# Optimization experiments

Hardware: AMD Instinct MI355X
Metric: run time of the kernel (lower is better)

Reference implementation:

```python
import jax, jax.numpy as jnp
import numpy as np

N = 100_000   # nodes
E = 1_600_000  # edges (avg degree 16)
D_IN, D_HID, D_OUT = 128, 128, 64


def setup_inputs() -> dict:
    key = jax.random.key(0)
    k = jax.random.split(key, 6)
    x = jax.random.normal(k[0], (N, D_IN), dtype=jnp.float32)
    edge_index = jax.random.randint(k[1], (2, E), 0, N, dtype=jnp.int32)
    W1 = jax.random.normal(k[2], (D_IN, D_HID), dtype=jnp.float32) / np.sqrt(D_IN)
    b1 = jnp.zeros((D_HID,), dtype=jnp.float32)
    W2 = jax.random.normal(k[3], (D_HID, D_OUT), dtype=jnp.float32) / np.sqrt(D_HID)
    b2 = jnp.zeros((D_OUT,), dtype=jnp.float32)
    return {"x": x, "edge_index": edge_index, "W1": W1, "b1": b1, "W2": W2, "b2": b2}


def reference(x, edge_index, W1, b1, W2, b2):
    # GCNConv (PyG defaults): add self-loops, symmetric deg^-1/2 normalization,
    # linear transform then sum-aggregate over neighbors, then bias.
    loop = jnp.arange(N, dtype=edge_index.dtype)
    src = jnp.concatenate([edge_index[0], loop])  # [E+N]
    dst = jnp.concatenate([edge_index[1], loop])  # [E+N]

    deg = jax.ops.segment_sum(jnp.ones(src.shape, jnp.float32), dst, num_segments=N)
    inv_sqrt_deg = jnp.where(deg > 0, jax.lax.rsqrt(jnp.maximum(deg, 1.0)), 0.0)
    coef = (inv_sqrt_deg[src] * inv_sqrt_deg[dst])[:, None]  # [E+N, 1]

    def gcn_conv(h, W, b):
        h = h @ W                                   # [N, d_out]
        msg = h[src] * coef                          # gather + scale, [E+N, d_out]
        return jax.ops.segment_sum(msg, dst, num_segments=N) + b

    h = jax.nn.relu(gcn_conv(x, W1, b1))
    # dropout is identity in eval mode
    return gcn_conv(h, W2, b2)
```

## Files before the change

### kernel.cpp

```cpp
#include <hip/hip_runtime.h>

#define NN 100000
#define NE 1600000
#define DI 128
#define DH 128
#define DO 64
#define NBK 391
#define SLOT 5120
#define PAD 16
#define EPB 8192
#define NSB ((NE + EPB - 1) / EPB)

typedef unsigned int uint;
typedef unsigned short ushort;
typedef __bf16 bf16x8 __attribute__((ext_vector_type(8)));
typedef float f32x4 __attribute__((ext_vector_type(4)));

__device__ __forceinline__ float bf_lo(uint u) { return __uint_as_float(u << 16); }
__device__ __forceinline__ float bf_hi(uint u) { return __uint_as_float(u & 0xffff0000u); }
__device__ __forceinline__ ushort f2bf(float f) {
    uint u = __float_as_uint(f);
    uint r = u + 0x7fffu + ((u >> 16) & 1u);
    return (ushort)(r >> 16);
}

__global__ void k_prep(const float* __restrict__ W1, const float* __restrict__ W2,
                       ushort* __restrict__ w1t, ushort* __restrict__ w2t,
                       int* __restrict__ bcur) {
    int t = blockIdx.x * 256 + threadIdx.x;
    if (t < NBK) bcur[t * PAD] = t * SLOT;
    if (t < 128 * 128) {
        int c = t >> 7, k = t & 127;
        w1t[t] = f2bf(W1[k * 128 + c]);
    } else if (t < 128 * 128 + 64 * 128) {
        int u = t - 128 * 128;
        int c = u >> 7, k = u & 127;
        w2t[u] = f2bf(W2[k * 64 + c]);
    }
}

__global__ __launch_bounds__(512) void k_bscatter(const int* __restrict__ src,
                                                  const int* __restrict__ dst,
                                                  int* __restrict__ bcur,
                                                  uint* __restrict__ ebuf) {
    __shared__ uint stage[EPB];
    __shared__ ushort bktid[EPB];
    __shared__ int lcnt[NBK];
    __shared__ int loff[NBK];
    __shared__ int gbase[NBK];
    __shared__ int s[512];
    int t = threadIdx.x;
    int e0 = blockIdx.x * EPB;
    int n = min(EPB, NE - e0);
    for (int i = t; i < NBK; i += 512) lcnt[i] = 0;
    __syncthreads();
    for (int i = t; i < n; i += 512)
        atomicAdd(&lcnt[dst[e0 + i] >> 8], 1);
    __syncthreads();
    int myc = (t < NBK) ? lcnt[t] : 0;
    s[t] = myc;
    __syncthreads();
    for (int d = 1; d < 512; d <<= 1) {
        int a = (t >= d) ? s[t - d] : 0;
        __syncthreads();
        s[t] += a;
        __syncthreads();
    }
    if (t < NBK) {
        loff[t] = s[t] - myc;
        gbase[t] = atomicAdd(&bcur[t * PAD], myc);
        lcnt[t] = s[t] - myc;
    }
    __syncthreads();
    for (int i = t; i < n; i += 512) {
        int d = dst[e0 + i];
        int sv = src[e0 + i];
        int b = d >> 8;
        int p = atomicAdd(&lcnt[b], 1);
        stage[p] = ((uint)sv << 8) | (uint)(d & 255);
        bktid[p] = (ushort)b;
    }
    __syncthreads();
    for (int j = t; j < n; j += 512) {
        int b = bktid[j];
        ebuf[gbase[b] + (j - loff[b])] = stage[j];
    }
}

__global__ __launch_bounds__(256) void k_bfill(const uint* __restrict__ ebuf,
                                               const int* __restrict__ bcur,
                                               uint2* __restrict__ offdeg,
                                               float* __restrict__ inv,
                                               int* __restrict__ csr_src) {
    __shared__ int cnt[256];
    __shared__ int s[256];
    __shared__ int cur[256];
    int b = blockIdx.x, t = threadIdx.x;
    int ebeg = b * SLOT;
    int eend = bcur[b * PAD];
    cnt[t] = 0;
    __syncthreads();
    for (int e = ebeg + t; e < eend; e += 256)
        atomicAdd(&cnt[ebuf[e] & 255], 1);
    __syncthreads();
    int v = cnt[t];
    s[t] = v;
    __syncthreads();
    for (int d = 1; d < 256; d <<= 1) {
        int a = (t >= d) ? s[t - d] : 0;
        __syncthreads();
        s[t] += a;
        __syncthreads();
    }
    int beg = ebeg + s[t] - v;
    int node = b * 256 + t;
    if (node < NN) {
        offdeg[node] = make_uint2((uint)beg, (uint)v);
        inv[node] = rsqrtf((float)v + 1.0f);
    }
    cur[t] = beg;
    __syncthreads();
    for (int e = ebeg + t; e < eend; e += 256) {
        uint ed = ebuf[e];
        int p = atomicAdd(&cur[ed & 255], 1);
        csr_src[p] = (int)(ed >> 8);
    }
}

template <int N, bool ABF16>
__global__ __launch_bounds__(256) void k_gemm_mfma(const void* __restrict__ Ap,
                                                   const ushort* __restrict__ Wt,
                                                   const float* __restrict__ inv,
                                                   ushort* __restrict__ out) {
    int wid = threadIdx.x >> 6;
    int lane = threadIdx.x & 63;
    int r0 = (blockIdx.x * 4 + wid) * 32;
    if (r0 >= NN) return;
    int rlo = lane & 15, khi = lane >> 4;

    constexpr int CT = N / 16;
    f32x4 acc[2][CT] = {};

#pragma unroll
    for (int ks = 0; ks < 4; ++ks) {
        bf16x8 bf[CT];
#pragma unroll
        for (int ct = 0; ct < CT; ++ct)
            bf[ct] = *(const bf16x8*)(Wt + (ct * 16 + rlo) * 128 + ks * 32 + khi * 8);
#pragma unroll
        for (int rt = 0; rt < 2; ++rt) {
            int row = r0 + rt * 16 + rlo;
            bf16x8 af;
            if (ABF16) {
                af = *(const bf16x8*)((const ushort*)Ap + (size_t)row * 128 + ks * 32 + khi * 8);
            } else {
                const float* pa = (const float*)Ap + (size_t)row * 128 + ks * 32 + khi * 8;
                float4 f0 = *(const float4*)pa;
                float4 f1 = *(const float4*)(pa + 4);
                af[0] = (__bf16)f0.x; af[1] = (__bf16)f0.y;
                af[2] = (__bf16)f0.z; af[3] = (__bf16)f0.w;
                af[4] = (__bf16)f1.x; af[5] = (__bf16)f1.y;
                af[6] = (__bf16)f1.z; af[7] = (__bf16)f1.w;
            }
#pragma unroll
            for (int ct = 0; ct < CT; ++ct)
                acc[rt][ct] = __builtin_amdgcn_mfma_f32_16x16x32_bf16(af, bf[ct], acc[rt][ct], 0, 0, 0);
        }
    }
#pragma unroll
    for (int rt = 0; rt < 2; ++rt) {
        int rowb = r0 + rt * 16 + 4 * khi;
#pragma unroll
        for (int b = 0; b < 4; ++b) {
            float sc = inv[rowb + b];
#pragma unroll
            for (int ct = 0; ct < CT; ++ct)
                out[(size_t)(rowb + b) * N + ct * 16 + rlo] = f2bf(acc[rt][ct][b] * sc);
        }
    }
}

template <bool RELU>
__global__ void k_agg128(const uint2* __restrict__ offdeg, const int* __restrict__ csr,
                         const ushort* __restrict__ tab, const float* __restrict__ inv,
                         const float* __restrict__ bias, ushort* __restrict__ outb) {
    int wid = threadIdx.x >> 6, lane = threadIdx.x & 63;
    int node = blockIdx.x * (blockDim.x >> 6) + wid;
    if (node >= NN) return;
    uint2 od = offdeg[node];
    int beg = (int)od.x, end = beg + (int)od.y;
    const uint* t32 = (const uint*)tab;
    float a0 = 0.f, a1 = 0.f;
    int e = beg;
    for (; e + 3 < end; e += 4) {
        int s0 = csr[e], s1 = csr[e + 1], s2 = csr[e + 2], s3 = csr[e + 3];
        uint u0 = t32[(size_t)s0 * 64 + lane];
        uint u1 = t32[(size_t)s1 * 64 + lane];
        uint u2 = t32[(size_t)s2 * 64 + lane];
        uint u3 = t32[(size_t)s3 * 64 + lane];
        a0 += bf_lo(u0); a1 += bf_hi(u0);
        a0 += bf_lo(u1); a1 += bf_hi(u1);
        a0 += bf_lo(u2); a1 += bf_hi(u2);
        a0 += bf_lo(u3); a1 += bf_hi(u3);
    }
    for (; e < end; ++e) {
        int s = csr[e];
        uint u = t32[(size_t)s * 64 + lane];
        a0 += bf_lo(u); a1 += bf_hi(u);
    }
    float invd = inv[node];
    uint us = t32[(size_t)node * 64 + lane];
    float2 b = *(const float2*)(bias + lane * 2);
    float r0 = fmaf(invd, a0 + bf_lo(us), b.x);
    float r1 = fmaf(invd, a1 + bf_hi(us), b.y);
    if (RELU) { r0 = fmaxf(r0, 0.f); r1 = fmaxf(r1, 0.f); }
    uint packed = (uint)f2bf(r0) | ((uint)f2bf(r1) << 16);
    *(uint*)(outb + (size_t)node * 128 + lane * 2) = packed;
}

__global__ void k_agg64(const uint2* __restrict__ offdeg, const int* __restrict__ csr,
                        const ushort* __restrict__ tab, const float* __restrict__ inv,
                        const float* __restrict__ bias, float* __restrict__ out) {
    int wid = threadIdx.x >> 6, lane = threadIdx.x & 63;
    int node = blockIdx.x * (blockDim.x >> 6) + wid;
    if (node >= NN) return;
    uint2 od = offdeg[node];
    int beg = (int)od.x, end = beg + (int)od.y;
    float a0 = 0.f;
    int e = beg;
    for (; e + 3 < end; e += 4) {
        int s0 = csr[e], s1 = csr[e + 1], s2 = csr[e + 2], s3 = csr[e + 3];
        float h0 = __uint_as_float((uint)tab[(size_t)s0 * 64 + lane] << 16);
        float h1 = __uint_as_float((uint)tab[(size_t)s1 * 64 + lane] << 16);
        float h2 = __uint_as_float((uint)tab[(size_t)s2 * 64 + lane] << 16);
        float h3 = __uint_as_float((uint)tab[(size_t)s3 * 64 + lane] << 16);
        a0 += h0; a0 += h1; a0 += h2; a0 += h3;
    }
    for (; e < end; ++e) {
        int s = csr[e];
        a0 += __uint_as_float((uint)tab[(size_t)s * 64 + lane] << 16);
    }
    float invd = inv[node];
    float hs = __uint_as_float((uint)tab[(size_t)node * 64 + lane] << 16);
    out[(size_t)node * 64 + lane] = fmaf(invd, a0 + hs, bias[lane]);
}

extern "C" void kernel_launch(void* const* d_in, const int* in_sizes, int n_in,
                              void* d_out, int out_size, void* d_ws, size_t ws_size,
                              hipStream_t stream) {
    const float* x  = (const float*)d_in[0];
    const int* ei   = (const int*)d_in[1];
    const int* src  = ei;
    const int* dst  = ei + NE;
    const float* W1 = (const float*)d_in[2];
    const float* b1 = (const float*)d_in[3];
    const float* W2 = (const float*)d_in[4];
    const float* b2 = (const float*)d_in[5];
    float* out = (float*)d_out;

    uint2*  offdeg  = (uint2*)d_ws;
    float*  inv     = (float*)(offdeg + NN);
    int*    bcur    = (int*)(inv + 100004);
    int*    csr_src = bcur + NBK * PAD;
    ushort* w1t     = (ushort*)(csr_src + NBK * SLOT);
    ushort* w2t     = w1t + 128 * 128;
    ushort* h       = w2t + 64 * 128;
    ushort* hagg    = h + (size_t)NN * DH;
    ushort* h2      = hagg + (size_t)NN * DH;
    uint*   ebuf    = (uint*)h2;

    k_prep<<<96, 256, 0, stream>>>(W1, W2, w1t, w2t, bcur);
    k_bscatter<<<NSB, 512, 0, stream>>>(src, dst, bcur, ebuf);
    k_bfill<<<NBK, 256, 0, stream>>>(ebuf, bcur, offdeg, inv, csr_src);

    k_gemm_mfma<DH, false><<<(NN + 127) / 128, 256, 0, stream>>>(x, w1t, inv, h);
    k_agg128<true><<<NN / 4, 256, 0, stream>>>(offdeg, csr_src, h, inv, b1, hagg);

    k_gemm_mfma<DO, true><<<(NN + 127) / 128, 256, 0, stream>>>(hagg, w2t, inv, h2);
    k_agg64<<<NN / 4, 256, 0, stream>>>(offdeg, csr_src, h2, inv, b2, out);
}
```

Measured before the change: 244.3 us.

## Store features in 16-column slices and aggregate per slice for cache locality

Intermediate bf16 feature tables now use a column-sliced layout: 16-column slices, each covering all nodes contiguously. Both GEMMs read and write this layout, and the aggregation kernels run one slice per block. Each slice covers only a few MB, so the random neighbour gathers for that slice should stay in L2/MALL cache instead of thrashing across the full table. Within a wavefront, lanes are split into 8-lane feature groups and 4 edge subgroups per node, reduced with shuffles. In exchange, each gather is a 32-byte segment rather than a full 256-byte row, and the CSR indices are re-read once per slice.

```diff
diff --git a/kernel.cpp b/kernel.cpp
--- a/kernel.cpp
+++ b/kernel.cpp
@@ -5,6 +5,7 @@
 #define DI 128
 #define DH 128
 #define DO 64
+#define NN16 ((size_t)NN * 16)
 #define NBK 391
 #define SLOT 5120
 #define PAD 16
@@ -152,7 +153,9 @@
             int row = r0 + rt * 16 + rlo;
             bf16x8 af;
             if (ABF16) {
-                af = *(const bf16x8*)((const ushort*)Ap + (size_t)row * 128 + ks * 32 + khi * 8);
+                const ushort* As = (const ushort*)Ap;
+                af = *(const bf16x8*)(As + (size_t)(2 * ks + (khi >> 1)) * NN16 +
+                                      (size_t)row * 16 + (khi & 1) * 8);
             } else {
                 const float* pa = (const float*)Ap + (size_t)row * 128 + ks * 32 + khi * 8;
                 float4 f0 = *(const float4*)pa;
@@ -175,74 +178,103 @@
             float sc = inv[rowb + b];
 #pragma unroll
             for (int ct = 0; ct < CT; ++ct)
-                out[(size_t)(rowb + b) * N + ct * 16 + rlo] = f2bf(acc[rt][ct][b] * sc);
-        }
-    }
-}
-
-template <bool RELU>
-__global__ void k_agg128(const uint2* __restrict__ offdeg, const int* __restrict__ csr,
-                         const ushort* __restrict__ tab, const float* __restrict__ inv,
-                         const float* __restrict__ bias, ushort* __restrict__ outb) {
+                out[(size_t)ct * NN16 + (size_t)(rowb + b) * 16 + rlo] = f2bf(acc[rt][ct][b] * sc);
+        }
+    }
+}
+
+__global__ __launch_bounds__(256) void k_aggs128(const uint2* __restrict__ offdeg,
+                                                 const int* __restrict__ csr,
+                                                 const ushort* __restrict__ tab,
+                                                 const float* __restrict__ inv,
+                                                 const float* __restrict__ bias,
+                                                 ushort* __restrict__ outb) {
+    int slice = blockIdx.x & 7;
+    int grp = blockIdx.x >> 3;
     int wid = threadIdx.x >> 6, lane = threadIdx.x & 63;
-    int node = blockIdx.x * (blockDim.x >> 6) + wid;
-    if (node >= NN) return;
-    uint2 od = offdeg[node];
-    int beg = (int)od.x, end = beg + (int)od.y;
-    const uint* t32 = (const uint*)tab;
-    float a0 = 0.f, a1 = 0.f;
-    int e = beg;
-    for (; e + 3 < end; e += 4) {
-        int s0 = csr[e], s1 = csr[e + 1], s2 = csr[e + 2], s3 = csr[e + 3];
-        uint u0 = t32[(size_t)s0 * 64 + lane];
-        uint u1 = t32[(size_t)s1 * 64 + lane];
-        uint u2 = t32[(size_t)s2 * 64 + lane];
-        uint u3 = t32[(size_t)s3 * 64 + lane];
-        a0 += bf_lo(u0); a1 += bf_hi(u0);
-        a0 += bf_lo(u1); a1 += bf_hi(u1);
-        a0 += bf_lo(u2); a1 += bf_hi(u2);
-        a0 += bf_lo(u3); a1 += bf_hi(u3);
-    }
-    for (; e < end; ++e) {
-        int s = csr[e];
-        uint u = t32[(size_t)s * 64 + lane];
-        a0 += bf_lo(u); a1 += bf_hi(u);
-    }
-    float invd = inv[node];
-    uint us = t32[(size_t)node * 64 + lane];
-    float2 b = *(const float2*)(bias + lane * 2);
-    float r0 = fmaf(invd, a0 + bf_lo(us), b.x);
-    float r1 = fmaf(invd, a1 + bf_hi(us), b.y);
-    if (RELU) { r0 = fmaxf(r0, 0.f); r1 = fmaxf(r1, 0.f); }
-    uint packed = (uint)f2bf(r0) | ((uint)f2bf(r1) << 16);
-    *(uint*)(outb + (size_t)node * 128 + lane * 2) = packed;
-}
-
-__global__ void k_agg64(const uint2* __restrict__ offdeg, const int* __restrict__ csr,
-                        const ushort* __restrict__ tab, const float* __restrict__ inv,
-                        const float* __restrict__ bias, float* __restrict__ out) {
+    int nsub = lane >> 5;
+    int esub = (lane >> 3) & 3;
+    int u = lane & 7;
+    const uint* t32 = (const uint*)(tab + (size_t)slice * NN16);
+    uint* o32 = (uint*)outb + (size_t)slice * (NN * 8);
+    float2 bb = *(const float2*)(bias + slice * 16 + u * 2);
+#pragma unroll
+    for (int half = 0; half < 2; ++half) {
+        int node = grp * 16 + half * 8 + wid * 2 + nsub;
+        uint2 od = offdeg[node];
+        int beg = (int)od.x, deg = (int)od.y;
+        float a0 = 0.f, a1 = 0.f;
+        int k = esub;
+        for (; k + 4 < deg; k += 8) {
+            int s0 = csr[beg + k];
+            int s1 = csr[beg + k + 4];
+            uint u0 = t32[s0 * 8 + u];
+            uint u1 = t32[s1 * 8 + u];
+            a0 += bf_lo(u0); a1 += bf_hi(u0);
+            a0 += bf_lo(u1); a1 += bf_hi(u1);
+        }
+        if (k < deg) {
+            int s0 = csr[beg + k];
+            uint u0 = t32[s0 * 8 + u];
+            a0 += bf_lo(u0); a1 += bf_hi(u0);
+        }
+        a0 += __shfl_xor(a0, 8); a0 += __shfl_xor(a0, 16);
+        a1 += __shfl_xor(a1, 8); a1 += __shfl_xor(a1, 16);
+        if (esub == 0) {
+            float invd = inv[node];
+            uint us = t32[node * 8 + u];
+            float r0 = fmaf(invd, a0 + bf_lo(us), bb.x);
+            float r1 = fmaf(invd, a1 + bf_hi(us), bb.y);
+            r0 = fmaxf(r0, 0.f); r1 = fmaxf(r1, 0.f);
+            o32[(size_t)node * 8 + u] = (uint)f2bf(r0) | ((uint)f2bf(r1) << 16);
+        }
+    }
+}
+
+__global__ __launch_bounds__(256) void k_aggs64(const uint2* __restrict__ offdeg,
+                                                const int* __restrict__ csr,
+                                                const ushort* __restrict__ tab,
+                                                const float* __restrict__ inv,
+                                                const float* __restrict__ bias,
+                                                float* __restrict__ out) {
+    int slice = blockIdx.x & 3;
+    int grp = blockIdx.x >> 2;
     int wid = threadIdx.x >> 6, lane = threadIdx.x & 63;
-    int node = blockIdx.x * (blockDim.x >> 6) + wid;
-    if (node >= NN) return;
-    uint2 od = offdeg[node];
-    int beg = (int)od.x, end = beg + (int)od.y;
-    float a0 = 0.f;
-    int e = beg;
-    for (; e + 3 < end; e += 4) {
-        int s0 = csr[e], s1 = csr[e + 1], s2 = csr[e + 2], s3 = csr[e + 3];
-        float h0 = __uint_as_float((uint)tab[(size_t)s0 * 64 + lane] << 16);
-        float h1 = __uint_as_float((uint)tab[(size_t)s1 * 64 + lane] << 16);
-        float h2 = __uint_as_float((uint)tab[(size_t)s2 * 64 + lane] << 16);
-        float h3 = __uint_as_float((uint)tab[(size_t)s3 * 64 + lane] << 16);
-        a0 += h0; a0 += h1; a0 += h2; a0 += h3;
-    }
-    for (; e < end; ++e) {
-        int s = csr[e];
-        a0 += __uint_as_float((uint)tab[(size_t)s * 64 + lane] << 16);
-    }
-    float invd = inv[node];
-    float hs = __uint_as_float((uint)tab[(size_t)node * 64 + lane] << 16);
-    out[(size_t)node * 64 + lane] = fmaf(invd, a0 + hs, bias[lane]);
+    int nsub = lane >> 5;
+    int esub = (lane >> 3) & 3;
+    int u = lane & 7;
+    const uint* t32 = (const uint*)(tab + (size_t)slice * NN16);
+    float2 bb = *(const float2*)(bias + slice * 16 + u * 2);
+#pragma unroll
+    for (int half = 0; half < 2; ++half) {
+        int node = grp * 16 + half * 8 + wid * 2 + nsub;
+        uint2 od = offdeg[node];
+        int beg = (int)od.x, deg = (int)od.y;
+        float a0 = 0.f, a1 = 0.f;
+        int k = esub;
+        for (; k + 4 < deg; k += 8) {
+            int s0 = csr[beg + k];
+            int s1 = csr[beg + k + 4];
+            uint u0 = t32[s0 * 8 + u];
+            uint u1 = t32[s1 * 8 + u];
+            a0 += bf_lo(u0); a1 += bf_hi(u0);
+            a0 += bf_lo(u1); a1 += bf_hi(u1);
+        }
+        if (k < deg) {
+            int s0 = csr[beg + k];
+            uint u0 = t32[s0 * 8 + u];
+            a0 += bf_lo(u0); a1 += bf_hi(u0);
+        }
+        a0 += __shfl_xor(a0, 8); a0 += __shfl_xor(a0, 16);
+        a1 += __shfl_xor(a1, 8); a1 += __shfl_xor(a1, 16);
+        if (esub == 0) {
+            float invd = inv[node];
+            uint us = t32[node * 8 + u];
+            float2 r = make_float2(fmaf(invd, a0 + bf_lo(us), bb.x),
+                                   fmaf(invd, a1 + bf_hi(us), bb.y));
+            *(float2*)(out + (size_t)node * 64 + slice * 16 + u * 2) = r;
+        }
+    }
 }
 
 extern "C" void kernel_launch(void* const* d_in, const int* in_sizes, int n_in,
@@ -274,8 +306,8 @@
     k_bfill<<<NBK, 256, 0, stream>>>(ebuf, bcur, offdeg, inv, csr_src);
 
     k_gemm_mfma<DH, false><<<(NN + 127) / 128, 256, 0, stream>>>(x, w1t, inv, h);
-    k_agg128<true><<<NN / 4, 256, 0, stream>>>(offdeg, csr_src, h, inv, b1, hagg);
+    k_aggs128<<<(NN / 16) * 8, 256, 0, stream>>>(offdeg, csr_src, h, inv, b1, hagg);
 
     k_gemm_mfma<DO, true><<<(NN + 127) / 128, 256, 0, stream>>>(hagg, w2t, inv, h2);
-    k_agg64<<<NN / 4, 256, 0, stream>>>(offdeg, csr_src, h2, inv, b2, out);
-}
+    k_aggs64<<<(NN / 16) * 4, 256, 0, stream>>>(offdeg, csr_src, h2, inv, b2, out);
+}
```

After: 294.2 us. 20.4% more time.
